# Kernel optimization log

Hardware: AMD Instinct MI355X
Metric: run time of the kernel (lower is better)

Reference implementation:

```python
import jax, jax.numpy as jnp
import numpy as np

B, S, D_IN, RANK, D_OUT = 8, 1024, 1280, 64, 1280
DOWN_SIZE = RANK * D_IN      # 81920
UP_SIZE = D_OUT * RANK       # 81920


def setup_inputs() -> dict:
    key = jax.random.key(0)
    k1, k2 = jax.random.split(key)
    x = jax.random.normal(k1, (B, S, D_IN), dtype=jnp.float32)
    # per-image embedding that encodes the dynamic LoRA weights
    embed = jax.random.normal(k2, (B, DOWN_SIZE + UP_SIZE), dtype=jnp.float32) * 0.02
    return {"x": x, "embed": embed}


def reference(x, embed):
    # down_forward: per-sample weight = embed[:, :down_size].view(down_shape)=[rank, d_in]
    # original does x_chunk @ W.T per sample; batched as a single grouped GEMM
    w_down = embed[:, :DOWN_SIZE].reshape(B, RANK, D_IN)   # [B, r, d_in]
    h = jnp.einsum('bsd,brd->bsr', x, w_down)              # x @ W_down.T, batched
    # up_forward: per-sample weight = embed[:, -up_size:].view(up_shape)=[d_out, rank]
    w_up = embed[:, -UP_SIZE:].reshape(B, D_OUT, RANK)     # [B, d_out, r]
    out = jnp.einsum('bsr,bor->bso', h, w_up)              # h @ W_up.T, batched
    return out
```

## Files before the change

kernel.cpp:

```cpp
#include <hip/hip_runtime.h>

#define NB   8
#define S_   1024
#define DIN  1280
#define RANK 64
#define DOUT 1280
#define DOWN (RANK * DIN)
#define EMB  (DOWN + DOUT * RANK)
#define XSTRIDE 1288

typedef __bf16 bf16x8 __attribute__((ext_vector_type(8)));
typedef __bf16 bf16x4 __attribute__((ext_vector_type(4)));
typedef float  f32x4  __attribute__((ext_vector_type(4)));

__global__ __launch_bounds__(256) void cvt_embed(const float* __restrict__ src,
                                                 __bf16* __restrict__ dst, int n8) {
    const int i = blockIdx.x * 256 + threadIdx.x;
    if (i < n8) {
        const float4* s = reinterpret_cast<const float4*>(src) + (size_t)i * 2;
        float4 f0 = s[0], f1 = s[1];
        bf16x8 v;
        v[0]=(__bf16)f0.x; v[1]=(__bf16)f0.y; v[2]=(__bf16)f0.z; v[3]=(__bf16)f0.w;
        v[4]=(__bf16)f1.x; v[5]=(__bf16)f1.y; v[6]=(__bf16)f1.z; v[7]=(__bf16)f1.w;
        *reinterpret_cast<bf16x8*>(dst + (size_t)i * 8) = v;
    }
}

__global__ __launch_bounds__(512, 2) void lora_main(const float* __restrict__ x,
                                                    const __bf16* __restrict__ ew,
                                                    float* __restrict__ out) {
    __shared__ __bf16 xls[16 * XSTRIDE];
    __shared__ float  pbuf[4][16][20];
    __shared__ __bf16 hld[16][80];

    const int b    = blockIdx.x & 7;
    const int s0   = (blockIdx.x >> 3) * 16;
    const int t    = threadIdx.x;
    const int w    = t >> 6;
    const int l    = t & 63;
    const int quad = l >> 4;
    const int lc   = l & 15;
    const int dq   = quad * 8;

    {
        const int row = t >> 5;
        const int c   = t & 31;
        const float4* src = reinterpret_cast<const float4*>(x + (size_t)(b * S_ + s0 + row) * DIN);
        __bf16* drow = xls + row * XSTRIDE;
#pragma unroll
        for (int j = 0; j < 10; ++j) {
            float4 f = src[c + 32 * j];
            bf16x4 v;
            v[0]=(__bf16)f.x; v[1]=(__bf16)f.y; v[2]=(__bf16)f.z; v[3]=(__bf16)f.w;
            *reinterpret_cast<bf16x4*>(drow + c * 4 + 128 * j) = v;
        }
    }
    __syncthreads();

    const int nt = w & 3;
    const int kh = w >> 2;
    const __bf16* wdrow  = ew + (size_t)b * EMB + (size_t)(nt * 16 + lc) * DIN + kh * 640;
    const __bf16* xlsrow = xls + lc * XSTRIDE + kh * 640;

    f32x4 acc = {0,0,0,0};
#pragma unroll 5
    for (int ks = 0; ks < 20; ++ks) {
        const int k = ks * 32 + dq;
        bf16x8 af = *reinterpret_cast<const bf16x8*>(xlsrow + k);
        bf16x8 bf = *reinterpret_cast<const bf16x8*>(wdrow + k);
        acc = __builtin_amdgcn_mfma_f32_16x16x32_bf16(af, bf, acc, 0, 0, 0);
    }

    if (kh == 1) {
#pragma unroll
        for (int i = 0; i < 4; ++i) pbuf[nt][quad * 4 + i][lc] = acc[i];
    }
    __syncthreads();
    if (kh == 0) {
#pragma unroll
        for (int i = 0; i < 4; ++i) {
            float v = acc[i] + pbuf[nt][quad * 4 + i][lc];
            hld[quad * 4 + i][nt * 16 + lc] = (__bf16)v;
        }
    }
    __syncthreads();

    bf16x8 ha0 = *reinterpret_cast<const bf16x8*>(&hld[lc][dq]);
    bf16x8 ha1 = *reinterpret_cast<const bf16x8*>(&hld[lc][32 + dq]);
    const __bf16* wu    = ew + (size_t)b * EMB + DOWN;
    float*        obase = out + (size_t)(b * S_ + s0 + quad * 4) * DOUT;

#pragma unroll 2
    for (int tt = 0; tt < 10; ++tt) {
        const int n = w + 8 * tt;
        const int o = n * 16 + lc;
        bf16x8 b0 = *reinterpret_cast<const bf16x8*>(wu + (size_t)o * RANK + dq);
        bf16x8 b1 = *reinterpret_cast<const bf16x8*>(wu + (size_t)o * RANK + 32 + dq);
        f32x4 c = {0,0,0,0};
        c = __builtin_amdgcn_mfma_f32_16x16x32_bf16(ha0, b0, c, 0, 0, 0);
        c = __builtin_amdgcn_mfma_f32_16x16x32_bf16(ha1, b1, c, 0, 0, 0);
#pragma unroll
        for (int i = 0; i < 4; ++i)
            obase[(size_t)i * DOUT + o] = c[i];
    }
}

extern "C" void kernel_launch(void* const* d_in, const int* in_sizes, int n_in,
                              void* d_out, int out_size, void* d_ws, size_t ws_size,
                              hipStream_t stream) {
    const float* x     = (const float*)d_in[0];
    const float* embed = (const float*)d_in[1];
    float*       out   = (float*)d_out;
    __bf16*      ew    = (__bf16*)d_ws;
    (void)in_sizes; (void)n_in; (void)out_size; (void)ws_size;

    cvt_embed<<<dim3(640), dim3(256), 0, stream>>>(embed, ew, NB * EMB / 8);
    lora_main<<<dim3(512), dim3(512), 0, stream>>>(x, ew, out);
}
```

Measured before the change: 110.5 us.

## Stage LoRA weights through swizzled double-buffered LDS via async global_load_lds

Both the down-projection and up-projection weight tiles are now streamed into a swizzled, double-buffered LDS region using direct global-to-LDS loads, with the next tile prefetched while MFMAs consume the current one. Previously each wave read the weights straight from global memory. The aim is to hide weight-load latency and make fragment reads conflict-free, at the cost of more LDS per block (~80KB), many extra barriers, and possibly lower occupancy.

New measurement: 100.3 us. 1.1x faster.

```diff
diff --git a/kernel.cpp b/kernel.cpp
--- a/kernel.cpp
+++ b/kernel.cpp
@@ -9,9 +9,25 @@
 #define EMB  (DOWN + DOUT * RANK)
 #define XSTRIDE 1288
 
+#define XLS_OFF   0
+#define XLS_BYTES (16 * XSTRIDE * 2)
+#define WB_OFF    XLS_BYTES
+#define WB_BYTES  (2 * 16384)
+#define PB_OFF    (WB_OFF + WB_BYTES)
+#define PB_BYTES  (4 * 16 * 17 * 4)
+#define HL_OFF    (PB_OFF + PB_BYTES)
+#define HL_BYTES  (16 * 80 * 2)
+#define LDS_TOTAL (HL_OFF + HL_BYTES)
+
 typedef __bf16 bf16x8 __attribute__((ext_vector_type(8)));
 typedef __bf16 bf16x4 __attribute__((ext_vector_type(4)));
 typedef float  f32x4  __attribute__((ext_vector_type(4)));
+
+#define GLOAD16(gsrc, ldsoff)                                              \
+    __builtin_amdgcn_global_load_lds(                                      \
+        (const __attribute__((address_space(1))) void*)(gsrc),             \
+        (__attribute__((address_space(3))) void*)(smem + (ldsoff)),        \
+        16, 0, 0)
 
 __global__ __launch_bounds__(256) void cvt_embed(const float* __restrict__ src,
                                                  __bf16* __restrict__ dst, int n8) {
@@ -29,9 +45,10 @@
 __global__ __launch_bounds__(512, 2) void lora_main(const float* __restrict__ x,
                                                     const __bf16* __restrict__ ew,
                                                     float* __restrict__ out) {
-    __shared__ __bf16 xls[16 * XSTRIDE];
-    __shared__ float  pbuf[4][16][20];
-    __shared__ __bf16 hld[16][80];
+    extern __shared__ char smem[];
+    __bf16* xls = (__bf16*)(smem + XLS_OFF);
+    float (*pbuf)[16][17] = (float(*)[16][17])(smem + PB_OFF);
+    __bf16 (*hld)[80]     = (__bf16(*)[80])(smem + HL_OFF);
 
     const int b    = blockIdx.x & 7;
     const int s0   = (blockIdx.x >> 3) * 16;
@@ -42,6 +59,25 @@
     const int lc   = l & 15;
     const int dq   = quad * 8;
 
+    const int nt = w & 3;
+    const int kh = w >> 2;
+
+    const char* wdB = (const char*)(ew + (size_t)b * EMB);
+    const char* wuB = wdB + (size_t)DOWN * 2;
+    const int d0 = w * 2048 + l * 16;
+    const int d1 = d0 + 1024;
+    const int kh0 = d0 >> 13,        kh1 = d1 >> 13;
+    const int r0  = (d0 >> 7) & 63,  r1  = (d1 >> 7) & 63;
+    const int cB0 = d0 & 127,        cB1 = d1 & 127;
+    const char* p1a = wdB + r0 * 2560 + kh0 * 1280 + (cB0 ^ ((r0 & 7) << 4));
+    const char* p1b = wdB + r1 * 2560 + kh1 * 1280 + (cB1 ^ ((r1 & 7) << 4));
+    const char* p2a = wuB + (d0 ^ (((d0 >> 7) & 7) << 4));
+    const char* p2b = wuB + (d1 ^ (((d1 >> 7) & 7) << 4));
+    const int ldsA = WB_OFF + w * 2048;
+    const int bswz = (lc & 7) << 4;
+
+    GLOAD16(p1a, ldsA);
+    GLOAD16(p1b, ldsA + 1024);
     {
         const int row = t >> 5;
         const int c   = t & 31;
@@ -57,18 +93,27 @@
     }
     __syncthreads();
 
-    const int nt = w & 3;
-    const int kh = w >> 2;
-    const __bf16* wdrow  = ew + (size_t)b * EMB + (size_t)(nt * 16 + lc) * DIN + kh * 640;
-    const __bf16* xlsrow = xls + lc * XSTRIDE + kh * 640;
-
+    const __bf16* xrow = xls + lc * XSTRIDE + kh * 640;
+    const int brow = kh * 8192 + (nt * 16 + lc) * 128;
     f32x4 acc = {0,0,0,0};
-#pragma unroll 5
-    for (int ks = 0; ks < 20; ++ks) {
-        const int k = ks * 32 + dq;
-        bf16x8 af = *reinterpret_cast<const bf16x8*>(xlsrow + k);
-        bf16x8 bf = *reinterpret_cast<const bf16x8*>(wdrow + k);
-        acc = __builtin_amdgcn_mfma_f32_16x16x32_bf16(af, bf, acc, 0, 0, 0);
+#pragma unroll
+    for (int c = 0; c < 10; ++c) {
+        const int nb = (c & 1) ^ 1;
+        if (c < 9) {
+            GLOAD16(p1a + (c + 1) * 128, nb * 16384 + ldsA);
+            GLOAD16(p1b + (c + 1) * 128, nb * 16384 + ldsA + 1024);
+        } else {
+            GLOAD16(p2a, ldsA);
+            GLOAD16(p2b, ldsA + 1024);
+        }
+        const char* bb = smem + WB_OFF + (c & 1) * 16384;
+#pragma unroll
+        for (int j = 0; j < 2; ++j) {
+            bf16x8 af = *reinterpret_cast<const bf16x8*>(xrow + c * 64 + j * 32 + dq);
+            bf16x8 bf = *reinterpret_cast<const bf16x8*>(bb + ((brow + j * 64 + quad * 16) ^ bswz));
+            acc = __builtin_amdgcn_mfma_f32_16x16x32_bf16(af, bf, acc, 0, 0, 0);
+        }
+        __syncthreads();
     }
 
     if (kh == 1) {
@@ -87,21 +132,27 @@
 
     bf16x8 ha0 = *reinterpret_cast<const bf16x8*>(&hld[lc][dq]);
     bf16x8 ha1 = *reinterpret_cast<const bf16x8*>(&hld[lc][32 + dq]);
-    const __bf16* wu    = ew + (size_t)b * EMB + DOWN;
-    float*        obase = out + (size_t)(b * S_ + s0 + quad * 4) * DOUT;
+    float* obase = out + (size_t)(b * S_ + s0 + quad * 4) * DOUT;
+    const int prow = (w * 16 + lc) * 128;
 
-#pragma unroll 2
+#pragma unroll
     for (int tt = 0; tt < 10; ++tt) {
-        const int n = w + 8 * tt;
-        const int o = n * 16 + lc;
-        bf16x8 b0 = *reinterpret_cast<const bf16x8*>(wu + (size_t)o * RANK + dq);
-        bf16x8 b1 = *reinterpret_cast<const bf16x8*>(wu + (size_t)o * RANK + 32 + dq);
-        f32x4 c = {0,0,0,0};
-        c = __builtin_amdgcn_mfma_f32_16x16x32_bf16(ha0, b0, c, 0, 0, 0);
-        c = __builtin_amdgcn_mfma_f32_16x16x32_bf16(ha1, b1, c, 0, 0, 0);
+        if (tt < 9) {
+            const int nb = (tt & 1) ^ 1;
+            GLOAD16(p2a + (tt + 1) * 16384, nb * 16384 + ldsA);
+            GLOAD16(p2b + (tt + 1) * 16384, nb * 16384 + ldsA + 1024);
+        }
+        const char* bb = smem + WB_OFF + (tt & 1) * 16384;
+        bf16x8 b0 = *reinterpret_cast<const bf16x8*>(bb + ((prow + quad * 16) ^ bswz));
+        bf16x8 b1 = *reinterpret_cast<const bf16x8*>(bb + ((prow + 64 + quad * 16) ^ bswz));
+        f32x4 c4 = {0,0,0,0};
+        c4 = __builtin_amdgcn_mfma_f32_16x16x32_bf16(ha0, b0, c4, 0, 0, 0);
+        c4 = __builtin_amdgcn_mfma_f32_16x16x32_bf16(ha1, b1, c4, 0, 0, 0);
+        const int o = (w + 8 * tt) * 16 + lc;
 #pragma unroll
         for (int i = 0; i < 4; ++i)
-            obase[(size_t)i * DOUT + o] = c[i];
+            obase[(size_t)i * DOUT + o] = c4[i];
+        if (tt < 9) __syncthreads();
     }
 }
 
@@ -115,5 +166,5 @@
     (void)in_sizes; (void)n_in; (void)out_size; (void)ws_size;
 
     cvt_embed<<<dim3(640), dim3(256), 0, stream>>>(embed, ew, NB * EMB / 8);
-    lora_main<<<dim3(512), dim3(512), 0, stream>>>(x, ew, out);
+    lora_main<<<dim3(512), dim3(512), LDS_TOTAL, stream>>>(x, ew, out);
 }
```
